# Optimization experiments

Measured on AMD Instinct MI355X. Metric: run time of the kernel, lower is better.

## Reference

```python
import jax, jax.numpy as jnp
import numpy as np

N = 1024      # num_nodes
D = 64        # node_embedding_dim
H = 64        # hidden_dim
LN_EPS = 1e-5


def setup_inputs() -> dict:
    key = jax.random.key(0)
    ks = jax.random.split(key, 6)
    node_embeddings = jax.random.normal(ks[0], (N, D), dtype=jnp.float32)
    valid_mask = jax.random.randint(ks[1], (N * N,), 0, 2).astype(jnp.float32)
    s1 = 1.0 / np.sqrt(2 * D)
    s2 = 1.0 / np.sqrt(H)
    W1 = jax.random.normal(ks[2], (2 * D, H), dtype=jnp.float32) * s1
    b1 = jnp.zeros((H,), jnp.float32)
    g1 = jnp.ones((H,), jnp.float32)
    be1 = jnp.zeros((H,), jnp.float32)
    W2 = jax.random.normal(ks[3], (H, H), dtype=jnp.float32) * s2
    b2 = jnp.zeros((H,), jnp.float32)
    g2 = jnp.ones((H,), jnp.float32)
    be2 = jnp.zeros((H,), jnp.float32)
    W3 = jax.random.normal(ks[4], (H, 1), dtype=jnp.float32) * s2
    b3 = jnp.zeros((1,), jnp.float32)
    return {
        "node_embeddings": node_embeddings, "valid_mask": valid_mask,
        "W1": W1, "b1": b1, "g1": g1, "be1": be1,
        "W2": W2, "b2": b2, "g2": g2, "be2": be2,
        "W3": W3, "b3": b3,
    }


def _layer_norm(x, g, b):
    m = jnp.mean(x, axis=-1, keepdims=True)
    v = jnp.mean((x - m) ** 2, axis=-1, keepdims=True)
    return (x - m) * jax.lax.rsqrt(v + LN_EPS) * g + b


def reference(node_embeddings, valid_mask, W1, b1, g1, be1, W2, b2, g2, be2, W3, b3):
    n, d = node_embeddings.shape
    # Build all ordered pairs (i, j): concat([emb_i, emb_j]) -> [n*n, 2d]
    src = jnp.broadcast_to(node_embeddings[:, None, :], (n, n, d))
    tgt = jnp.broadcast_to(node_embeddings[None, :, :], (n, n, d))
    e = jnp.concatenate([src, tgt], axis=-1).reshape(n * n, 2 * d)
    # MLP: Linear -> LayerNorm -> ReLU (x2 hidden) -> Linear(1)
    h = jax.nn.relu(_layer_norm(e @ W1 + b1, g1, be1))
    h = jax.nn.relu(_layer_norm(h @ W2 + b2, g2, be2))
    scores = (h @ W3 + b3)[:, 0]  # [n*n]
    # Original never scores self-edges (i == j) and multiplies by valid_mask.
    off_diag = 1.0 - jnp.eye(n, dtype=scores.dtype).reshape(-1)
    return scores * valid_mask * off_diag
```

## Files before the change

kernel.cpp:

```cpp
#include <hip/hip_runtime.h>
#include <hip/hip_bf16.h>

#define NN 1024
#define LN_EPS 1e-5f

typedef __bf16 bf16x8 __attribute__((ext_vector_type(8)));
typedef float floatx4 __attribute__((ext_vector_type(4)));
typedef float floatx2 __attribute__((ext_vector_type(2)));

__global__ void precompute_ab(const float* __restrict__ emb, const float* __restrict__ W1,
                              const float* __restrict__ b1, const float* __restrict__ W2,
                              float* __restrict__ Ap, float* __restrict__ Bt,
                              float* __restrict__ sumA, float* __restrict__ sumB,
                              __bf16* __restrict__ Wf) {
    if (blockIdx.x == 1024) {
        int lane = threadIdx.x;
        int m_l = lane & 15, kg = lane >> 4;
#pragma unroll
        for (int mt = 0; mt < 4; mt++)
#pragma unroll
            for (int kc = 0; kc < 2; kc++) {
                bf16x8 f;
#pragma unroll
                for (int t = 0; t < 8; t++) {
                    int k = kc * 32 + kg * 8 + t;
                    f[t] = (__bf16)W2[k * 64 + mt * 16 + m_l];
                }
                *(bf16x8*)&Wf[((mt * 2 + kc) * 64 + lane) * 8] = f;
            }
        return;
    }
    __shared__ __align__(16) float e[64];
    int i = blockIdx.x, h = threadIdx.x;
    e[h] = emb[i * 64 + h];
    __syncthreads();
    float a = b1[h], b = 0.f;
#pragma unroll
    for (int d = 0; d < 64; d++) {
        a = fmaf(e[d], W1[d * 64 + h], a);
        b = fmaf(e[d], W1[(64 + d) * 64 + h], b);
    }
    Ap[i * 64 + h] = a;
    Bt[h * NN + i] = b;
    float ra = a, rb = b;
#pragma unroll
    for (int off = 1; off < 64; off <<= 1) {
        ra += __shfl_xor(ra, off);
        rb += __shfl_xor(rb, off);
    }
    if (h == 0) { sumA[i] = ra; sumB[i] = rb; }
}

__global__ __launch_bounds__(256, 4) void fused(
    const float* __restrict__ Ap, const float* __restrict__ Bt, const __bf16* __restrict__ Wf,
    const float* __restrict__ sumA, const float* __restrict__ sumB,
    const float* __restrict__ g1, const float* __restrict__ be1, const float* __restrict__ b2,
    const float* __restrict__ g2, const float* __restrict__ be2, const float* __restrict__ W3,
    const float* __restrict__ b3, const float* __restrict__ mask, float* __restrict__ out) {
    __shared__ __align__(16) float Arow[64], G1[64], BE1[64], B2s[64], G2s[64], BE2s[64], W3s[64];
    __shared__ __align__(16) __bf16 h1t[4][64 * 64];

    int tid = threadIdx.x;
    int wave = tid >> 6, lane = tid & 63;
    int i = blockIdx.x >> 2;
    int j0 = (blockIdx.x & 3) * 256 + wave * 64;

    if (tid < 64) {
        Arow[tid] = Ap[i * 64 + tid];
        G1[tid] = g1[tid];  BE1[tid] = be1[tid];
        B2s[tid] = b2[tid]; G2s[tid] = g2[tid]; BE2s[tid] = be2[tid];
        W3s[tid] = W3[tid];
    }
    __syncthreads();

    int m_l = lane & 15, kg = lane >> 4;

    bf16x8 afrag[4][2];
#pragma unroll
    for (int mt = 0; mt < 4; mt++)
#pragma unroll
        for (int kc = 0; kc < 2; kc++)
            afrag[mt][kc] = *(const bf16x8*)&Wf[((mt * 2 + kc) * 64 + lane) * 8];

    float sBj = sumB[j0 + lane];
    const float* btp = Bt + j0 + lane;
    floatx2 x2[32];
    floatx2 qa = {0.f, 0.f}, qb = {0.f, 0.f};
#pragma unroll
    for (int h2 = 0; h2 < 32; h2++) {
        floatx2 bb = { btp[(2 * h2) * NN], btp[(2 * h2 + 1) * NN] };
        floatx2 aa = *(const floatx2*)&Arow[2 * h2];
        floatx2 v = aa + bb;
        x2[h2] = v;
        if (h2 & 1) qb += v * v;
        else        qa += v * v;
    }
    floatx2 qs = qa + qb;
    float sq = qs[0] + qs[1];
    float m1 = (sumA[i] + sBj) * 0.015625f;
    float var1 = fmaf(m1, -m1, sq * 0.015625f);
    float rs1 = rsqrtf(var1 + LN_EPS);
    floatx2 p1 = {rs1, rs1};
    float ofs = -m1 * rs1;
    floatx2 o1 = {ofs, ofs};

    __bf16* rowp = &h1t[wave][lane * 64];
    int sw = lane & 7;
#pragma unroll
    for (int c = 0; c < 8; c++) {
        bf16x8 fr;
#pragma unroll
        for (int t = 0; t < 4; t++) {
            floatx2 gg = *(const floatx2*)&G1[c * 8 + 2 * t];
            floatx2 ee = *(const floatx2*)&BE1[c * 8 + 2 * t];
            floatx2 xn = x2[c * 4 + t] * p1 + o1;
            floatx2 y  = xn * gg + ee;
            y = __builtin_elementwise_max(y, (floatx2){0.f, 0.f});
            fr[2 * t]     = (__bf16)y[0];
            fr[2 * t + 1] = (__bf16)y[1];
        }
        *(bf16x8*)(rowp + ((c ^ sw) * 8)) = fr;
    }
    asm volatile("s_waitcnt lgkmcnt(0)" ::: "memory");

    floatx4 acc[4][4];
#pragma unroll
    for (int a = 0; a < 4; a++)
#pragma unroll
        for (int b = 0; b < 4; b++) acc[a][b] = (floatx4){0.f, 0.f, 0.f, 0.f};

    const __bf16* wbase = &h1t[wave][0];
#pragma unroll
    for (int nt = 0; nt < 4; nt++) {
        int pair = nt * 16 + m_l;
#pragma unroll
        for (int kc = 0; kc < 2; kc++) {
            int chunk = kc * 4 + kg;
            bf16x8 bfrag = *(const bf16x8*)(wbase + pair * 64 + ((chunk ^ (pair & 7)) * 8));
#pragma unroll
            for (int mt = 0; mt < 4; mt++)
                acc[mt][nt] =
                    __builtin_amdgcn_mfma_f32_16x16x32_bf16(afrag[mt][kc], bfrag, acc[mt][nt], 0, 0, 0);
        }
    }

    float b3v = b3[0];

#pragma unroll
    for (int nt = 0; nt < 4; nt++) {
        floatx2 s2v = {0.f, 0.f}, q2v = {0.f, 0.f};
#pragma unroll
        for (int mt = 0; mt < 4; mt++) {
            floatx2 blo = *(const floatx2*)&B2s[mt * 16 + kg * 4];
            floatx2 bhi = *(const floatx2*)&B2s[mt * 16 + kg * 4 + 2];
            floatx2 vlo = { acc[mt][nt][0], acc[mt][nt][1] };
            floatx2 vhi = { acc[mt][nt][2], acc[mt][nt][3] };
            vlo += blo; vhi += bhi;
            acc[mt][nt][0] = vlo[0]; acc[mt][nt][1] = vlo[1];
            acc[mt][nt][2] = vhi[0]; acc[mt][nt][3] = vhi[1];
            s2v += vlo; s2v += vhi;
            q2v += vlo * vlo; q2v += vhi * vhi;
        }
        float s2 = s2v[0] + s2v[1];
        float q2 = q2v[0] + q2v[1];
        s2 += __shfl_xor(s2, 16); s2 += __shfl_xor(s2, 32);
        q2 += __shfl_xor(q2, 16); q2 += __shfl_xor(q2, 32);
        float m2 = s2 * 0.015625f;
        float var2 = fmaf(m2, -m2, q2 * 0.015625f);
        float rs2 = rsqrtf(var2 + LN_EPS);
        floatx2 p2 = {rs2, rs2};
        float o2s = -m2 * rs2;
        floatx2 o2 = {o2s, o2s};

        floatx2 scv = {0.f, 0.f};
#pragma unroll
        for (int mt = 0; mt < 4; mt++) {
#pragma unroll
            for (int hh = 0; hh < 2; hh++) {
                floatx2 g = *(const floatx2*)&G2s[mt * 16 + kg * 4 + 2 * hh];
                floatx2 e = *(const floatx2*)&BE2s[mt * 16 + kg * 4 + 2 * hh];
                floatx2 w = *(const floatx2*)&W3s[mt * 16 + kg * 4 + 2 * hh];
                floatx2 v = { acc[mt][nt][2 * hh], acc[mt][nt][2 * hh + 1] };
                floatx2 xn = v * p2 + o2;
                floatx2 y  = xn * g + e;
                y = __builtin_elementwise_max(y, (floatx2){0.f, 0.f});
                scv += y * w;
            }
        }
        float sc = scv[0] + scv[1];
        sc += __shfl_xor(sc, 16); sc += __shfl_xor(sc, 32);

        if (kg == 0) {
            int j = j0 + nt * 16 + m_l;
            int p = i * NN + j;
            out[p] = (i == j) ? 0.f : (sc + b3v) * mask[p];
        }
    }
}

extern "C" void kernel_launch(void* const* d_in, const int* in_sizes, int n_in,
                              void* d_out, int out_size, void* d_ws, size_t ws_size,
                              hipStream_t stream) {
    const float* emb = (const float*)d_in[0];
    const float* mask = (const float*)d_in[1];
    const float* W1 = (const float*)d_in[2];
    const float* b1 = (const float*)d_in[3];
    const float* g1 = (const float*)d_in[4];
    const float* be1 = (const float*)d_in[5];
    const float* W2 = (const float*)d_in[6];
    const float* b2 = (const float*)d_in[7];
    const float* g2 = (const float*)d_in[8];
    const float* be2 = (const float*)d_in[9];
    const float* W3 = (const float*)d_in[10];
    const float* b3 = (const float*)d_in[11];
    float* out = (float*)d_out;

    float* Ap = (float*)d_ws;
    float* Bt = Ap + 1024 * 64;
    float* sA = Bt + 64 * 1024;
    float* sB = sA + 1024;
    __bf16* Wf = (__bf16*)(sB + 1024);

    precompute_ab<<<1025, 64, 0, stream>>>(emb, W1, b1, W2, Ap, Bt, sA, sB, Wf);
    fused<<<4096, 256, 0, stream>>>(Ap, Bt, Wf, sA, sB, g1, be1, b2, g2, be2, W3, b3, mask, out);
}
```

Before: 116.1 us.

## Switch second layer to 32x32x16 MFMA and use row-major B projections

Replaces the 16x16x32 bf16 MFMA tiling of the hidden-layer GEMM with 32x32x16 tiles, reorganizing the weight fragments, accumulators and LayerNorm reductions (fewer cross-lane shuffles). The B projection is stored row-major so each lane reads its 64 values with vector loads, in place of strided column loads from the transposed layout. g1/be1/Arow are now read directly from global memory and not staged in shared memory. The precompute kernel splits the dot product across four waves with a shared-memory reduction. The larger accumulator tile raises register pressure under the existing launch bounds, and per-lane row reads of B are uncoalesced across lanes.

```diff
diff --git a/kernel.cpp b/kernel.cpp
--- a/kernel.cpp
+++ b/kernel.cpp
@@ -5,59 +5,71 @@
 #define LN_EPS 1e-5f
 
 typedef __bf16 bf16x8 __attribute__((ext_vector_type(8)));
+typedef float floatx16 __attribute__((ext_vector_type(16)));
 typedef float floatx4 __attribute__((ext_vector_type(4)));
 typedef float floatx2 __attribute__((ext_vector_type(2)));
 
-__global__ void precompute_ab(const float* __restrict__ emb, const float* __restrict__ W1,
-                              const float* __restrict__ b1, const float* __restrict__ W2,
-                              float* __restrict__ Ap, float* __restrict__ Bt,
-                              float* __restrict__ sumA, float* __restrict__ sumB,
-                              __bf16* __restrict__ Wf) {
+__global__ __launch_bounds__(256) void precompute_ab(
+    const float* __restrict__ emb, const float* __restrict__ W1,
+    const float* __restrict__ b1, const float* __restrict__ W2,
+    float* __restrict__ Ap, float* __restrict__ Bp,
+    float* __restrict__ sumA, float* __restrict__ sumB,
+    __bf16* __restrict__ Wf) {
     if (blockIdx.x == 1024) {
-        int lane = threadIdx.x;
-        int m_l = lane & 15, kg = lane >> 4;
-#pragma unroll
-        for (int mt = 0; mt < 4; mt++)
-#pragma unroll
-            for (int kc = 0; kc < 2; kc++) {
+        int tid = threadIdx.x;
+        if (tid >= 64) return;
+        int m_l = tid & 31, kg = tid >> 5;
+#pragma unroll
+        for (int mt = 0; mt < 2; mt++)
+#pragma unroll
+            for (int s = 0; s < 4; s++) {
                 bf16x8 f;
 #pragma unroll
                 for (int t = 0; t < 8; t++) {
-                    int k = kc * 32 + kg * 8 + t;
-                    f[t] = (__bf16)W2[k * 64 + mt * 16 + m_l];
+                    int k = s * 16 + kg * 8 + t;
+                    f[t] = (__bf16)W2[k * 64 + mt * 32 + m_l];
                 }
-                *(bf16x8*)&Wf[((mt * 2 + kc) * 64 + lane) * 8] = f;
+                *(bf16x8*)&Wf[((mt * 4 + s) * 64 + tid) * 8] = f;
             }
         return;
     }
     __shared__ __align__(16) float e[64];
-    int i = blockIdx.x, h = threadIdx.x;
-    e[h] = emb[i * 64 + h];
+    __shared__ float pA[4][64], pB[4][64];
+    int i = blockIdx.x;
+    int h = threadIdx.x & 63, q = threadIdx.x >> 6;
+    if (threadIdx.x < 64) e[h] = emb[i * 64 + h];
     __syncthreads();
-    float a = b1[h], b = 0.f;
-#pragma unroll
-    for (int d = 0; d < 64; d++) {
+    float a = 0.f, b = 0.f;
+#pragma unroll
+    for (int dd = 0; dd < 16; dd++) {
+        int d = q * 16 + dd;
         a = fmaf(e[d], W1[d * 64 + h], a);
         b = fmaf(e[d], W1[(64 + d) * 64 + h], b);
     }
-    Ap[i * 64 + h] = a;
-    Bt[h * NN + i] = b;
-    float ra = a, rb = b;
-#pragma unroll
-    for (int off = 1; off < 64; off <<= 1) {
-        ra += __shfl_xor(ra, off);
-        rb += __shfl_xor(rb, off);
-    }
-    if (h == 0) { sumA[i] = ra; sumB[i] = rb; }
+    pA[q][h] = a;
+    pB[q][h] = b;
+    __syncthreads();
+    if (threadIdx.x < 64) {
+        float ra = pA[0][h] + pA[1][h] + pA[2][h] + pA[3][h] + b1[h];
+        float rb = pB[0][h] + pB[1][h] + pB[2][h] + pB[3][h];
+        Ap[i * 64 + h] = ra;
+        Bp[i * 64 + h] = rb;
+#pragma unroll
+        for (int off = 1; off < 64; off <<= 1) {
+            ra += __shfl_xor(ra, off);
+            rb += __shfl_xor(rb, off);
+        }
+        if (h == 0) { sumA[i] = ra; sumB[i] = rb; }
+    }
 }
 
 __global__ __launch_bounds__(256, 4) void fused(
-    const float* __restrict__ Ap, const float* __restrict__ Bt, const __bf16* __restrict__ Wf,
+    const float* __restrict__ Ap, const float* __restrict__ Bp, const __bf16* __restrict__ Wf,
     const float* __restrict__ sumA, const float* __restrict__ sumB,
     const float* __restrict__ g1, const float* __restrict__ be1, const float* __restrict__ b2,
     const float* __restrict__ g2, const float* __restrict__ be2, const float* __restrict__ W3,
     const float* __restrict__ b3, const float* __restrict__ mask, float* __restrict__ out) {
-    __shared__ __align__(16) float Arow[64], G1[64], BE1[64], B2s[64], G2s[64], BE2s[64], W3s[64];
+    __shared__ __align__(16) float B2s[64], G2s[64], BE2s[64], W3s[64];
     __shared__ __align__(16) __bf16 h1t[4][64 * 64];
 
     int tid = threadIdx.x;
@@ -66,34 +78,27 @@
     int j0 = (blockIdx.x & 3) * 256 + wave * 64;
 
     if (tid < 64) {
-        Arow[tid] = Ap[i * 64 + tid];
-        G1[tid] = g1[tid];  BE1[tid] = be1[tid];
-        B2s[tid] = b2[tid]; G2s[tid] = g2[tid]; BE2s[tid] = be2[tid];
-        W3s[tid] = W3[tid];
+        B2s[tid] = b2[tid]; G2s[tid] = g2[tid];
+        BE2s[tid] = be2[tid]; W3s[tid] = W3[tid];
     }
     __syncthreads();
 
-    int m_l = lane & 15, kg = lane >> 4;
-
-    bf16x8 afrag[4][2];
-#pragma unroll
-    for (int mt = 0; mt < 4; mt++)
-#pragma unroll
-        for (int kc = 0; kc < 2; kc++)
-            afrag[mt][kc] = *(const bf16x8*)&Wf[((mt * 2 + kc) * 64 + lane) * 8];
-
-    float sBj = sumB[j0 + lane];
-    const float* btp = Bt + j0 + lane;
+    int j = j0 + lane;
+    float sBj = sumB[j];
+    const floatx4* bp4 = (const floatx4*)(Bp + j * 64);
+    const floatx4* ap4 = (const floatx4*)(Ap + i * 64);
     floatx2 x2[32];
     floatx2 qa = {0.f, 0.f}, qb = {0.f, 0.f};
 #pragma unroll
-    for (int h2 = 0; h2 < 32; h2++) {
-        floatx2 bb = { btp[(2 * h2) * NN], btp[(2 * h2 + 1) * NN] };
-        floatx2 aa = *(const floatx2*)&Arow[2 * h2];
-        floatx2 v = aa + bb;
-        x2[h2] = v;
-        if (h2 & 1) qb += v * v;
-        else        qa += v * v;
+    for (int c = 0; c < 16; c++) {
+        floatx4 bb = bp4[c];
+        floatx4 aa = ap4[c];
+        floatx2 v0 = {aa[0] + bb[0], aa[1] + bb[1]};
+        floatx2 v1 = {aa[2] + bb[2], aa[3] + bb[3]};
+        x2[2 * c] = v0;
+        x2[2 * c + 1] = v1;
+        qa += v0 * v0;
+        qb += v1 * v1;
     }
     floatx2 qs = qa + qb;
     float sq = qs[0] + qs[1];
@@ -111,60 +116,72 @@
         bf16x8 fr;
 #pragma unroll
         for (int t = 0; t < 4; t++) {
-            floatx2 gg = *(const floatx2*)&G1[c * 8 + 2 * t];
-            floatx2 ee = *(const floatx2*)&BE1[c * 8 + 2 * t];
+            floatx2 gg = *(const floatx2*)&g1[c * 8 + 2 * t];
+            floatx2 ee = *(const floatx2*)&be1[c * 8 + 2 * t];
             floatx2 xn = x2[c * 4 + t] * p1 + o1;
-            floatx2 y  = xn * gg + ee;
+            floatx2 y = xn * gg + ee;
             y = __builtin_elementwise_max(y, (floatx2){0.f, 0.f});
-            fr[2 * t]     = (__bf16)y[0];
+            fr[2 * t] = (__bf16)y[0];
             fr[2 * t + 1] = (__bf16)y[1];
         }
         *(bf16x8*)(rowp + ((c ^ sw) * 8)) = fr;
     }
     asm volatile("s_waitcnt lgkmcnt(0)" ::: "memory");
 
-    floatx4 acc[4][4];
-#pragma unroll
-    for (int a = 0; a < 4; a++)
-#pragma unroll
-        for (int b = 0; b < 4; b++) acc[a][b] = (floatx4){0.f, 0.f, 0.f, 0.f};
+    int m_l = lane & 31, kg2 = lane >> 5;
+    bf16x8 afrag[2][4];
+#pragma unroll
+    for (int mt = 0; mt < 2; mt++)
+#pragma unroll
+        for (int s = 0; s < 4; s++)
+            afrag[mt][s] = *(const bf16x8*)&Wf[((mt * 4 + s) * 64 + lane) * 8];
+
+    floatx16 acc[2][2];
+#pragma unroll
+    for (int a = 0; a < 2; a++)
+#pragma unroll
+        for (int b = 0; b < 2; b++)
+#pragma unroll
+            for (int r = 0; r < 16; r++) acc[a][b][r] = 0.f;
 
     const __bf16* wbase = &h1t[wave][0];
 #pragma unroll
-    for (int nt = 0; nt < 4; nt++) {
-        int pair = nt * 16 + m_l;
-#pragma unroll
-        for (int kc = 0; kc < 2; kc++) {
-            int chunk = kc * 4 + kg;
+    for (int nt = 0; nt < 2; nt++) {
+        int pair = nt * 32 + m_l;
+#pragma unroll
+        for (int s = 0; s < 4; s++) {
+            int chunk = s * 2 + kg2;
             bf16x8 bfrag = *(const bf16x8*)(wbase + pair * 64 + ((chunk ^ (pair & 7)) * 8));
 #pragma unroll
-            for (int mt = 0; mt < 4; mt++)
-                acc[mt][nt] =
-                    __builtin_amdgcn_mfma_f32_16x16x32_bf16(afrag[mt][kc], bfrag, acc[mt][nt], 0, 0, 0);
+            for (int mt = 0; mt < 2; mt++)
+                acc[mt][nt] = __builtin_amdgcn_mfma_f32_32x32x16_bf16(
+                    afrag[mt][s], bfrag, acc[mt][nt], 0, 0, 0);
         }
     }
 
     float b3v = b3[0];
 
 #pragma unroll
-    for (int nt = 0; nt < 4; nt++) {
+    for (int nt = 0; nt < 2; nt++) {
         floatx2 s2v = {0.f, 0.f}, q2v = {0.f, 0.f};
 #pragma unroll
-        for (int mt = 0; mt < 4; mt++) {
-            floatx2 blo = *(const floatx2*)&B2s[mt * 16 + kg * 4];
-            floatx2 bhi = *(const floatx2*)&B2s[mt * 16 + kg * 4 + 2];
-            floatx2 vlo = { acc[mt][nt][0], acc[mt][nt][1] };
-            floatx2 vhi = { acc[mt][nt][2], acc[mt][nt][3] };
-            vlo += blo; vhi += bhi;
-            acc[mt][nt][0] = vlo[0]; acc[mt][nt][1] = vlo[1];
-            acc[mt][nt][2] = vhi[0]; acc[mt][nt][3] = vhi[1];
-            s2v += vlo; s2v += vhi;
-            q2v += vlo * vlo; q2v += vhi * vhi;
+        for (int mt = 0; mt < 2; mt++) {
+#pragma unroll
+            for (int q = 0; q < 4; q++) {
+                int r0 = mt * 32 + q * 8 + kg2 * 4;
+                floatx4 bq = *(const floatx4*)&B2s[r0];
+                floatx2 vlo = {acc[mt][nt][q * 4 + 0] + bq[0], acc[mt][nt][q * 4 + 1] + bq[1]};
+                floatx2 vhi = {acc[mt][nt][q * 4 + 2] + bq[2], acc[mt][nt][q * 4 + 3] + bq[3]};
+                acc[mt][nt][q * 4 + 0] = vlo[0]; acc[mt][nt][q * 4 + 1] = vlo[1];
+                acc[mt][nt][q * 4 + 2] = vhi[0]; acc[mt][nt][q * 4 + 3] = vhi[1];
+                s2v += vlo; s2v += vhi;
+                q2v += vlo * vlo; q2v += vhi * vhi;
+            }
         }
         float s2 = s2v[0] + s2v[1];
         float q2 = q2v[0] + q2v[1];
-        s2 += __shfl_xor(s2, 16); s2 += __shfl_xor(s2, 32);
-        q2 += __shfl_xor(q2, 16); q2 += __shfl_xor(q2, 32);
+        s2 += __shfl_xor(s2, 32);
+        q2 += __shfl_xor(q2, 32);
         float m2 = s2 * 0.015625f;
         float var2 = fmaf(m2, -m2, q2 * 0.015625f);
         float rs2 = rsqrtf(var2 + LN_EPS);
@@ -174,26 +191,32 @@
 
         floatx2 scv = {0.f, 0.f};
 #pragma unroll
-        for (int mt = 0; mt < 4; mt++) {
-#pragma unroll
-            for (int hh = 0; hh < 2; hh++) {
-                floatx2 g = *(const floatx2*)&G2s[mt * 16 + kg * 4 + 2 * hh];
-                floatx2 e = *(const floatx2*)&BE2s[mt * 16 + kg * 4 + 2 * hh];
-                floatx2 w = *(const floatx2*)&W3s[mt * 16 + kg * 4 + 2 * hh];
-                floatx2 v = { acc[mt][nt][2 * hh], acc[mt][nt][2 * hh + 1] };
-                floatx2 xn = v * p2 + o2;
-                floatx2 y  = xn * g + e;
-                y = __builtin_elementwise_max(y, (floatx2){0.f, 0.f});
-                scv += y * w;
+        for (int mt = 0; mt < 2; mt++) {
+#pragma unroll
+            for (int q = 0; q < 4; q++) {
+                int r0 = mt * 32 + q * 8 + kg2 * 4;
+                floatx4 gq = *(const floatx4*)&G2s[r0];
+                floatx4 eq = *(const floatx4*)&BE2s[r0];
+                floatx4 wq = *(const floatx4*)&W3s[r0];
+                floatx2 vlo = {acc[mt][nt][q * 4 + 0], acc[mt][nt][q * 4 + 1]};
+                floatx2 vhi = {acc[mt][nt][q * 4 + 2], acc[mt][nt][q * 4 + 3]};
+                floatx2 xlo = vlo * p2 + o2;
+                floatx2 xhi = vhi * p2 + o2;
+                floatx2 ylo = xlo * (floatx2){gq[0], gq[1]} + (floatx2){eq[0], eq[1]};
+                floatx2 yhi = xhi * (floatx2){gq[2], gq[3]} + (floatx2){eq[2], eq[3]};
+                ylo = __builtin_elementwise_max(ylo, (floatx2){0.f, 0.f});
+                yhi = __builtin_elementwise_max(yhi, (floatx2){0.f, 0.f});
+                scv += ylo * (floatx2){wq[0], wq[1]};
+                scv += yhi * (floatx2){wq[2], wq[3]};
             }
         }
         float sc = scv[0] + scv[1];
-        sc += __shfl_xor(sc, 16); sc += __shfl_xor(sc, 32);
-
-        if (kg == 0) {
-            int j = j0 + nt * 16 + m_l;
-            int p = i * NN + j;
-            out[p] = (i == j) ? 0.f : (sc + b3v) * mask[p];
+        sc += __shfl_xor(sc, 32);
+
+        if (kg2 == 0) {
+            int jj = j0 + nt * 32 + m_l;
+            int p = i * NN + jj;
+            out[p] = (i == jj) ? 0.f : (sc + b3v) * mask[p];
         }
     }
 }
@@ -216,11 +239,11 @@
     float* out = (float*)d_out;
 
     float* Ap = (float*)d_ws;
-    float* Bt = Ap + 1024 * 64;
-    float* sA = Bt + 64 * 1024;
+    float* Bp = Ap + 1024 * 64;
+    float* sA = Bp + 1024 * 64;
     float* sB = sA + 1024;
     __bf16* Wf = (__bf16*)(sB + 1024);
 
-    precompute_ab<<<1025, 64, 0, stream>>>(emb, W1, b1, W2, Ap, Bt, sA, sB, Wf);
-    fused<<<4096, 256, 0, stream>>>(Ap, Bt, Wf, sA, sB, g1, be1, b2, g2, be2, W3, b3, mask, out);
+    precompute_ab<<<1025, 256, 0, stream>>>(emb, W1, b1, W2, Ap, Bp, sA, sB, Wf);
+    fused<<<4096, 256, 0, stream>>>(Ap, Bp, Wf, sA, sB, g1, be1, b2, g2, be2, W3, b3, mask, out);
 }
```

New measurement: 123.3 us. 1.06x slower.
